# Performance work log

Measured on AMD Instinct MI355X. Metric: run time of the kernel, lower is better.

The kernel has to match this reference:

```python
import jax, jax.numpy as jnp
import numpy as np

NUM_GROUPS = 64
TOPK = 8
BLOCK_M = 128
NUM_TOKENS = 8192
HIDDEN = 4096


def _build_perm(flat_ids_np, num_groups, block_m):
    """Single-pass histogram + stable sort + per-expert padding.

    Returns sorted_token_ids (int64, [total_padded]) and m_indices (int32,
    [total_padded]) exactly matching the torch per-expert loop semantics:
    each expert's slot list padded to a multiple of block_m by repeating its
    last slot (or zeros for empty experts).
    Output length is data-dependent, so this runs on host numpy (concrete
    values), mirroring the original module whose output shape is also
    data-dependent.
    """
    n = flat_ids_np.shape[0]
    order = np.argsort(flat_ids_np, kind="stable")  # token slots grouped by expert
    counts = np.bincount(flat_ids_np, minlength=num_groups)
    padded = (counts + block_m - 1) // block_m * block_m
    in_starts = np.concatenate([[0], np.cumsum(counts)])
    out_starts = np.concatenate([[0], np.cumsum(padded)])
    total = int(out_starts[-1])
    sorted_token_ids = np.zeros(total, dtype=np.int64)
    m_indices = np.zeros(total, dtype=np.int32)
    for e in range(num_groups):  # fixed small expert count
        c, p, o = int(counts[e]), int(padded[e]), int(out_starts[e])
        m_indices[o:o + p] = e
        if c > 0:
            seg = order[int(in_starts[e]):int(in_starts[e]) + c]
            sorted_token_ids[o:o + c] = seg
            sorted_token_ids[o + c:o + p] = seg[-1]  # pad with last slot
        # empty expert: rows stay zero (matches torch.zeros branch)
    np.clip(sorted_token_ids, None, n - 1, out=sorted_token_ids)
    return sorted_token_ids, m_indices


def setup_inputs() -> dict:
    key = jax.random.key(0)
    k1, k2 = jax.random.split(key)
    hidden_states = jax.random.normal(k1, (NUM_TOKENS, HIDDEN), dtype=jnp.bfloat16)
    topk_ids = jax.random.randint(k2, (NUM_TOKENS, TOPK), 0, NUM_GROUPS, dtype=jnp.int32)
    return {"hidden_states": hidden_states, "topk_ids": topk_ids}


def reference(hidden_states, topk_ids):
    m, _ = hidden_states.shape
    num_flat = m * TOPK
    flat_ids = np.asarray(topk_ids).reshape(-1)
    sorted_token_ids_np, m_indices_np = _build_perm(flat_ids, NUM_GROUPS, BLOCK_M)
    sorted_token_ids = jnp.asarray(sorted_token_ids_np)
    m_indices = jnp.asarray(m_indices_np)
    # inverse permutation for later unpermute (stable argsort breaks pad ties deterministically)
    inv_perm = jnp.argsort(sorted_token_ids, stable=True)[:num_flat]
    source_token_idx = sorted_token_ids // TOPK  # expert-contiguous gather indices
    output = hidden_states[source_token_idx]     # [total_padded, HIDDEN] bf16 gather
    return output, m_indices, inv_perm
```

## Files before the change

kernel.cpp:

```cpp
#include <hip/hip_runtime.h>
#include <hip/hip_bf16.h>

#define NG 64
#define TOPK 8
#define BM 128
#define NSLOT 65536
#define HID 4096
#define NTOK 8192
#define NSEG 64

typedef unsigned int v4u __attribute__((ext_vector_type(4)));


__global__ __launch_bounds__(256) void hist_k(const int* __restrict__ ids,
                                              int* __restrict__ ws) {
    __shared__ int h[NG], lm[NG];
    int t = threadIdx.x, s = blockIdx.x;
    if (t < NG) { h[t] = 0; lm[t] = -1; }
    __syncthreads();
    int base = s * 1024;
    for (int i = t; i < 1024; i += 256) {
        int e = ids[base + i] & (NG - 1);
        atomicAdd(&h[e], 1);
        atomicMax(&lm[e], base + i);
    }
    __syncthreads();
    if (t < NG) {
        ws[320 + t * 64 + s] = h[t];
        ws[4416 + t * 64 + s] = lm[t];
    }
}

__global__ __launch_bounds__(64) void scan_k(int* __restrict__ ws) {
    int e = threadIdx.x;
    int c = 0, last = -1;
    for (int b = 0; b < NSEG; b++) {
        c += ws[320 + e * 64 + b];
        int l = ws[4416 + e * 64 + b];
        last = l > last ? l : last;
    }
    ws[64 + e] = c;
    ws[128 + e] = (c + BM - 1) / BM * BM;
    ws[192 + e] = last;
    __syncthreads();
    if (e == 0) {
        int acc = 0;
        for (int f = 0; f < NG; f++) { ws[f] = acc; acc += ws[128 + f]; }
        ws[256] = acc;
    }
    __syncthreads();
    int acc = 0;
    for (int b = 0; b < NSEG; b++) {
        int sc = ws[320 + e * 64 + b];
        ws[320 + e * 64 + b] = acc;
        acc += sc;
    }
}

__global__ __launch_bounds__(64) void rank_k(const int* __restrict__ ids,
                                             const int* __restrict__ ws,
                                             unsigned short* __restrict__ rank) {
    int s = blockIdx.x;
    int lane = threadIdx.x;
    int base = ws[320 + lane * 64 + s];
    int segbase = s * 1024;
    unsigned long long below = (1ULL << lane) - 1ULL;
    for (int c0 = 0; c0 < 1024; c0 += 64) {
        int e = ids[segbase + c0 + lane] & (NG - 1);
        int r = 0;
#pragma unroll 8
        for (int x = 0; x < NG; x++) {
            unsigned long long m = __ballot(e == x);
            if (m) {
                int bx = __shfl(base, x);
                if (e == x) r = bx + __popcll(m & below);
                if (lane == x) base += (int)__popcll(m);
            }
        }
        rank[segbase + c0 + lane] = (unsigned short)r;
    }
}

__global__ __launch_bounds__(256) void inv_k(const int* __restrict__ ids,
                                             const int* __restrict__ ws,
                                             const unsigned short* __restrict__ rank,
                                             float* __restrict__ out) {
    __shared__ int s_last[NG], s_pad[NG];
    int t = threadIdx.x;
    if (t < NG) {
        s_last[t] = ws[192 + t];
        s_pad[t] = ws[128 + t] - ws[64 + t];
    }
    __syncthreads();
    int total = ws[256];
    float* inv_out = out + (size_t)total * (HID + 1);
    int i = blockIdx.x * 256 + t;
    int e = ids[i] & (NG - 1);
    int pos = ws[e] + (int)rank[i];
    int base = i;
#pragma unroll
    for (int f = 0; f < NG; f++) {
        int l = s_last[f];
        base += (l >= 0 && l < i) ? s_pad[f] : 0;
    }
    if (base < NSLOT) inv_out[base] = (float)pos;
    if (i == s_last[e]) {
        int oc = ws[e] + ws[64 + e];
        int pd = s_pad[e];
        for (int j = 0; j < pd; j++) {
            int idx = base + 1 + j;
            if (idx >= NSLOT) break;
            inv_out[idx] = (float)(oc + j);
        }
    }
}

__global__ __launch_bounds__(256) void copy_k(const __hip_bfloat16* __restrict__ hs,
                                              const int* __restrict__ ids,
                                              const int* __restrict__ ws,
                                              const unsigned short* __restrict__ rank,
                                              float* __restrict__ out) {
    int b = blockIdx.x;
    int total = ws[256];
    int t = threadIdx.x;
    float* m_out = out + (size_t)total * HID;
    if (b < NTOK) {
        const v4u* s = (const v4u*)(hs + (size_t)b * HID);
        v4u w0 = s[t];
        v4u w1 = s[t + 256];
        v4u a0 = {w0.x << 16, w0.x & 0xFFFF0000u, w0.y << 16, w0.y & 0xFFFF0000u};
        v4u a1 = {w0.z << 16, w0.z & 0xFFFF0000u, w0.w << 16, w0.w & 0xFFFF0000u};
        v4u a2 = {w1.x << 16, w1.x & 0xFFFF0000u, w1.y << 16, w1.y & 0xFFFF0000u};
        v4u a3 = {w1.z << 16, w1.z & 0xFFFF0000u, w1.w << 16, w1.w & 0xFFFF0000u};
        int slot0 = b * TOPK;
#pragma unroll
        for (int k = 0; k < TOPK; k++) {
            int e = ids[slot0 + k] & (NG - 1);
            int dst = ws[e] + (int)rank[slot0 + k];
            if (dst < 0 || dst >= total) continue;
            v4u* d = (v4u*)(out + (size_t)dst * HID);
            d[2 * t] = a0;
            d[2 * t + 1] = a1;
            d[2 * (t + 256)] = a2;
            d[2 * (t + 256) + 1] = a3;
            if (t == 0) m_out[dst] = (float)e;
        }
    } else {
        int q = b - NTOK;
        int e = q >> 7;
        int j = q & 127;
        int c = ws[64 + e], p = ws[128 + e];
        if (c + j >= p) return;
        int srcslot = ws[192 + e];
        int dst = ws[e] + c + j;
        if (dst < 0 || dst >= total) return;
        int src = srcslot >> 3;
        if (src < 0 || src >= NTOK) return;
        if (t == 0) m_out[dst] = (float)e;
        const v4u* s = (const v4u*)(hs + (size_t)src * HID);
        v4u* d = (v4u*)(out + (size_t)dst * HID);
#pragma unroll
        for (int half = 0; half < 2; half++) {
            int v = half * 256 + t;
            v4u w = s[v];
            v4u o1 = {w.x << 16, w.x & 0xFFFF0000u, w.y << 16, w.y & 0xFFFF0000u};
            v4u o2 = {w.z << 16, w.z & 0xFFFF0000u, w.w << 16, w.w & 0xFFFF0000u};
            d[2 * v] = o1;
            d[2 * v + 1] = o2;
        }
    }
}

extern "C" void kernel_launch(void* const* d_in, const int* in_sizes, int n_in,
                              void* d_out, int out_size, void* d_ws, size_t ws_size,
                              hipStream_t stream) {
    const __hip_bfloat16* hs = (const __hip_bfloat16*)d_in[0];
    const int* ids = (const int*)d_in[1];
    float* out = (float*)d_out;

    int* ws = (int*)d_ws;
    unsigned short* rank = (unsigned short*)(ws + 8704);

    hipLaunchKernelGGL(hist_k, dim3(NSEG), dim3(256), 0, stream, ids, ws);
    hipLaunchKernelGGL(scan_k, dim3(1), dim3(64), 0, stream, ws);
    hipLaunchKernelGGL(rank_k, dim3(NSEG), dim3(64), 0, stream, ids, ws, rank);
    hipLaunchKernelGGL(inv_k, dim3(NSLOT / 256), dim3(256), 0, stream, ids, ws, rank, out);
    hipLaunchKernelGGL(copy_k, dim3(NTOK + NG * BM), dim3(256), 0, stream,
                       hs, ids, ws, rank, out);
}
```

Baseline: 308.7 us.

## Fuse histogram with last-block scan and fold inverse-permutation into copy kernel

Merges the histogram and scan kernels using an atomic ticket so the last finishing block computes the per-expert totals and offsets. The per-segment prefix is now recomputed inside rank_k, and the inverse-permutation kernel becomes extra blocks of the copy kernel. This cuts the launch count from five to three and removes the serial scan launch. The risk is that the ticket counter in the workspace is never reset, and correctness relies on it wrapping modulo 64 across calls.

```diff
diff --git a/kernel.cpp b/kernel.cpp
--- a/kernel.cpp
+++ b/kernel.cpp
@@ -12,9 +12,10 @@
 typedef unsigned int v4u __attribute__((ext_vector_type(4)));
 
 
-__global__ __launch_bounds__(256) void hist_k(const int* __restrict__ ids,
-                                              int* __restrict__ ws) {
+__global__ __launch_bounds__(256) void hist_scan_k(const int* __restrict__ ids,
+                                                   int* __restrict__ ws) {
     __shared__ int h[NG], lm[NG];
+    __shared__ int winner;
     int t = threadIdx.x, s = blockIdx.x;
     if (t < NG) { h[t] = 0; lm[t] = -1; }
     __syncthreads();
@@ -29,31 +30,31 @@
         ws[320 + t * 64 + s] = h[t];
         ws[4416 + t * 64 + s] = lm[t];
     }
-}
-
-__global__ __launch_bounds__(64) void scan_k(int* __restrict__ ws) {
-    int e = threadIdx.x;
-    int c = 0, last = -1;
-    for (int b = 0; b < NSEG; b++) {
-        c += ws[320 + e * 64 + b];
-        int l = ws[4416 + e * 64 + b];
-        last = l > last ? l : last;
+    __threadfence();
+    __syncthreads();
+    if (t == 0) {
+        unsigned old = atomicAdd((unsigned*)&ws[257], 1u);
+        winner = ((old & 63u) == 63u) ? 1 : 0;
     }
-    ws[64 + e] = c;
-    ws[128 + e] = (c + BM - 1) / BM * BM;
-    ws[192 + e] = last;
     __syncthreads();
-    if (e == 0) {
+    if (!winner) return;
+    __threadfence();
+    if (t < NG) {
+        int e = t, c = 0, last = -1;
+        for (int b = 0; b < NSEG; b++) {
+            c += ws[320 + e * 64 + b];
+            int l = ws[4416 + e * 64 + b];
+            last = l > last ? l : last;
+        }
+        ws[64 + e] = c;
+        ws[128 + e] = (c + BM - 1) / BM * BM;
+        ws[192 + e] = last;
+    }
+    __syncthreads();
+    if (t == 0) {
         int acc = 0;
         for (int f = 0; f < NG; f++) { ws[f] = acc; acc += ws[128 + f]; }
         ws[256] = acc;
-    }
-    __syncthreads();
-    int acc = 0;
-    for (int b = 0; b < NSEG; b++) {
-        int sc = ws[320 + e * 64 + b];
-        ws[320 + e * 64 + b] = acc;
-        acc += sc;
     }
 }
 
@@ -62,7 +63,8 @@
                                              unsigned short* __restrict__ rank) {
     int s = blockIdx.x;
     int lane = threadIdx.x;
-    int base = ws[320 + lane * 64 + s];
+    int base = 0;
+    for (int s2 = 0; s2 < s; s2++) base += ws[320 + lane * 64 + s2];
     int segbase = s * 1024;
     unsigned long long below = (1ULL << lane) - 1ULL;
     for (int c0 = 0; c0 < 1024; c0 += 64) {
@@ -81,45 +83,12 @@
     }
 }
 
-__global__ __launch_bounds__(256) void inv_k(const int* __restrict__ ids,
-                                             const int* __restrict__ ws,
-                                             const unsigned short* __restrict__ rank,
-                                             float* __restrict__ out) {
-    __shared__ int s_last[NG], s_pad[NG];
-    int t = threadIdx.x;
-    if (t < NG) {
-        s_last[t] = ws[192 + t];
-        s_pad[t] = ws[128 + t] - ws[64 + t];
-    }
-    __syncthreads();
-    int total = ws[256];
-    float* inv_out = out + (size_t)total * (HID + 1);
-    int i = blockIdx.x * 256 + t;
-    int e = ids[i] & (NG - 1);
-    int pos = ws[e] + (int)rank[i];
-    int base = i;
-#pragma unroll
-    for (int f = 0; f < NG; f++) {
-        int l = s_last[f];
-        base += (l >= 0 && l < i) ? s_pad[f] : 0;
-    }
-    if (base < NSLOT) inv_out[base] = (float)pos;
-    if (i == s_last[e]) {
-        int oc = ws[e] + ws[64 + e];
-        int pd = s_pad[e];
-        for (int j = 0; j < pd; j++) {
-            int idx = base + 1 + j;
-            if (idx >= NSLOT) break;
-            inv_out[idx] = (float)(oc + j);
-        }
-    }
-}
-
 __global__ __launch_bounds__(256) void copy_k(const __hip_bfloat16* __restrict__ hs,
                                               const int* __restrict__ ids,
                                               const int* __restrict__ ws,
                                               const unsigned short* __restrict__ rank,
                                               float* __restrict__ out) {
+    __shared__ int s_last[NG], s_pad[NG];
     int b = blockIdx.x;
     int total = ws[256];
     int t = threadIdx.x;
@@ -145,7 +114,7 @@
             d[2 * (t + 256) + 1] = a3;
             if (t == 0) m_out[dst] = (float)e;
         }
-    } else {
+    } else if (b < NTOK + NG * BM) {
         int q = b - NTOK;
         int e = q >> 7;
         int j = q & 127;
@@ -168,6 +137,32 @@
             d[2 * v] = o1;
             d[2 * v + 1] = o2;
         }
+    } else {
+        if (t < NG) {
+            s_last[t] = ws[192 + t];
+            s_pad[t] = ws[128 + t] - ws[64 + t];
+        }
+        __syncthreads();
+        float* inv_out = out + (size_t)total * (HID + 1);
+        int i = (b - NTOK - NG * BM) * 256 + t;
+        int e = ids[i] & (NG - 1);
+        int pos = ws[e] + (int)rank[i];
+        int base = i;
+#pragma unroll
+        for (int f = 0; f < NG; f++) {
+            int l = s_last[f];
+            base += (l >= 0 && l < i) ? s_pad[f] : 0;
+        }
+        if (base < NSLOT) inv_out[base] = (float)pos;
+        if (i == s_last[e]) {
+            int oc = ws[e] + ws[64 + e];
+            int pd = s_pad[e];
+            for (int j = 0; j < pd; j++) {
+                int idx = base + 1 + j;
+                if (idx >= NSLOT) break;
+                inv_out[idx] = (float)(oc + j);
+            }
+        }
     }
 }
 
@@ -181,10 +176,8 @@
     int* ws = (int*)d_ws;
     unsigned short* rank = (unsigned short*)(ws + 8704);
 
-    hipLaunchKernelGGL(hist_k, dim3(NSEG), dim3(256), 0, stream, ids, ws);
-    hipLaunchKernelGGL(scan_k, dim3(1), dim3(64), 0, stream, ws);
+    hipLaunchKernelGGL(hist_scan_k, dim3(NSEG), dim3(256), 0, stream, ids, ws);
     hipLaunchKernelGGL(rank_k, dim3(NSEG), dim3(64), 0, stream, ids, ws, rank);
-    hipLaunchKernelGGL(inv_k, dim3(NSLOT / 256), dim3(256), 0, stream, ids, ws, rank, out);
-    hipLaunchKernelGGL(copy_k, dim3(NTOK + NG * BM), dim3(256), 0, stream,
+    hipLaunchKernelGGL(copy_k, dim3(NTOK + NG * BM + NSLOT / 256), dim3(256), 0, stream,
                        hs, ids, ws, rank, out);
 }
```

Measured after the change: 303.9 us. About the same (-1.6%).
